# Kernel optimization log

Hardware: AMD Instinct MI355X
Metric: run time of the kernel (lower is better)

Reference implementation:

```python
import jax, jax.numpy as jnp
import numpy as np

N_ITERS = 2
N_NODES = 50000
N_EDGES = 400000
NODE_DIM = 128
EDGE_DIM = 128
MLP_HIDDEN = 128


def _gru_cell(x, h, W_ih, W_hh, b_ih, b_hh):
    # torch.nn.GRUCell math. W_ih: [3H, in], W_hh: [3H, H]
    gi = x @ W_ih.T + b_ih
    gh = h @ W_hh.T + b_hh
    i_r, i_z, i_n = jnp.split(gi, 3, axis=-1)
    h_r, h_z, h_n = jnp.split(gh, 3, axis=-1)
    r = jax.nn.sigmoid(i_r + h_r)
    z = jax.nn.sigmoid(i_z + h_z)
    n = jnp.tanh(i_n + r * h_n)
    return (1.0 - z) * n + z * h


def _edge_softmax(logits, dst, num_nodes):
    # logits: [E], normalized over incoming edges of each dst node
    m = jax.ops.segment_max(logits, dst, num_segments=num_nodes)
    e = jnp.exp(logits - m[dst])
    s = jax.ops.segment_sum(e, dst, num_segments=num_nodes)
    return e / s[dst]


def setup_inputs() -> dict:
    key = jax.random.key(0)
    ks = jax.random.split(key, 20)
    s = 0.05
    inp = {
        'nf': jax.random.normal(ks[0], (N_NODES, NODE_DIM), jnp.float32),
        'ef': jax.random.normal(ks[1], (N_EDGES, EDGE_DIM), jnp.float32),
        'src': jax.random.randint(ks[2], (N_EDGES,), 0, N_NODES, jnp.int32),
        'dst': jax.random.randint(ks[3], (N_EDGES,), 0, N_NODES, jnp.int32),
        # edge GRUCell: input 2*node_dim -> hidden edge_dim
        'eW_ih': s * jax.random.normal(ks[4], (3 * EDGE_DIM, 2 * NODE_DIM), jnp.float32),
        'eW_hh': s * jax.random.normal(ks[5], (3 * EDGE_DIM, EDGE_DIM), jnp.float32),
        'eb_ih': s * jax.random.normal(ks[6], (3 * EDGE_DIM,), jnp.float32),
        'eb_hh': s * jax.random.normal(ks[7], (3 * EDGE_DIM,), jnp.float32),
        # node GRUCell: input edge_dim -> hidden node_dim
        'nW_ih': s * jax.random.normal(ks[8], (3 * NODE_DIM, EDGE_DIM), jnp.float32),
        'nW_hh': s * jax.random.normal(ks[9], (3 * NODE_DIM, NODE_DIM), jnp.float32),
        'nb_ih': s * jax.random.normal(ks[10], (3 * NODE_DIM,), jnp.float32),
        'nb_hh': s * jax.random.normal(ks[11], (3 * NODE_DIM,), jnp.float32),
        # attention MLP: edge_dim -> hidden -> 1
        'aW1': s * jax.random.normal(ks[12], (EDGE_DIM, MLP_HIDDEN), jnp.float32),
        'ab1': jnp.zeros((MLP_HIDDEN,), jnp.float32),
        'aW2': s * jax.random.normal(ks[13], (MLP_HIDDEN, 1), jnp.float32),
        'ab2': jnp.zeros((1,), jnp.float32),
    }
    return inp


def reference(nf, ef, src, dst, eW_ih, eW_hh, eb_ih, eb_hh,
              nW_ih, nW_hh, nb_ih, nb_hh, aW1, ab1, aW2, ab2):
    num_nodes = nf.shape[0]
    for _ in range(N_ITERS):
        # per-edge GRU update: input = [src_h ; dst_h], hidden = edge feature
        x_e = jnp.concatenate([nf[src], nf[dst]], axis=-1)  # [E, 2*node_dim]
        uef = _gru_cell(x_e, ef, eW_ih, eW_hh, eb_ih, eb_hh)  # [E, edge_dim]
        # attention MLP + edge softmax over destination neighborhoods
        logits = (jax.nn.relu(uef @ aW1 + ab1) @ aW2 + ab2)[:, 0]  # [E]
        attn = _edge_softmax(logits, dst, num_nodes)  # [E]
        # weighted scatter-sum aggregation to destination nodes
        agg_m = jax.ops.segment_sum(uef * attn[:, None], dst, num_segments=num_nodes)
        # node GRU update
        unf = _gru_cell(agg_m, nf, nW_ih, nW_hh, nb_ih, nb_hh)  # [N, node_dim]
        nf, ef = unf, uef
    return (nf, ef)
```

## Files before the change

### kernel.cpp

```cpp
#include <hip/hip_runtime.h>

#define NN 50000
#define NE 400000
#define DIM 128

typedef __bf16 bf16x8 __attribute__((ext_vector_type(8)));
typedef float f32x4 __attribute__((ext_vector_type(4)));
typedef unsigned short u16;

#define MFMA16 __builtin_amdgcn_mfma_f32_16x16x32_bf16

__device__ __forceinline__ u16 f2b(float f){ __bf16 b=(__bf16)f; return __builtin_bit_cast(u16,b); }
__device__ __forceinline__ float b2f(u16 h){ unsigned u = ((unsigned)h)<<16; return __builtin_bit_cast(float,u); }
__device__ __forceinline__ float sigm(float x){ return 1.0f/(1.0f+__expf(-x)); }
__device__ __forceinline__ float tanh_(float x){ float e=__expf(2.0f*x); return 1.0f-2.0f/(e+1.0f); }
__device__ __forceinline__ bf16x8 ldb8(const u16* p){ return *reinterpret_cast<const bf16x8*>(p); }

#define GLOAD_LDS(gp, lp) __builtin_amdgcn_global_load_lds( \
    (const __attribute__((address_space(1))) void*)(gp),    \
    (__attribute__((address_space(3))) void*)(lp), 16, 0, 0)

__global__ void f2b_kernel(const float* __restrict__ in, u16* __restrict__ out, int n4){
  int i = blockIdx.x*blockDim.x + threadIdx.x;
  int st = gridDim.x*blockDim.x;
  for (; i<n4; i+=st){
    float4 v = reinterpret_cast<const float4*>(in)[i];
    ushort4 o = { f2b(v.x), f2b(v.y), f2b(v.z), f2b(v.w) };
    reinterpret_cast<ushort4*>(out)[i] = o;
  }
}

__global__ void transpose128_kernel(const float* __restrict__ in, u16* __restrict__ out){
  int i = blockIdx.x*blockDim.x + threadIdx.x;
  int k = i>>7, n = i&127;
  out[n*128+k] = f2b(in[i]);
}

__global__ void zero_kernel(int* p, int n){
  int i = blockIdx.x*blockDim.x + threadIdx.x; if (i<n) p[i]=0;
}
__global__ void hist_kernel(const int* __restrict__ dst, int* __restrict__ counts, int n){
  int i = blockIdx.x*blockDim.x + threadIdx.x; if (i<n) atomicAdd(&counts[dst[i]],1);
}
__global__ void scan_kernel(const int* __restrict__ counts, int* __restrict__ rowp,
                            int* __restrict__ cursor, int n){
  __shared__ int buf[1024];
  __shared__ int run;
  const int t = threadIdx.x;
  if (t==0) run = 0;
  __syncthreads();
  for (int base=0; base<n; base+=1024){
    int v = (base+t<n) ? counts[base+t] : 0;
    buf[t]=v; __syncthreads();
    for (int off=1; off<1024; off<<=1){
      int x = (t>=off) ? buf[t-off] : 0;
      __syncthreads();
      buf[t]+=x; __syncthreads();
    }
    int incl = buf[t];
    int br = run;
    __syncthreads();
    if (base+t<n){ int ex = br+incl-v; rowp[base+t]=ex; cursor[base+t]=ex; }
    if (t==1023) run = br+incl;
    __syncthreads();
  }
  if (t==0) rowp[n]=run;
}
__global__ void scatter_kernel(const int* __restrict__ dst, int* __restrict__ cursor,
                               int* __restrict__ eids, int n){
  int i = blockIdx.x*blockDim.x + threadIdx.x;
  if (i<n){ int p = atomicAdd(&cursor[dst[i]],1); eids[p]=i; }
}

__global__ __launch_bounds__(512, 4)
void edge_kernel(const int* __restrict__ src, const int* __restrict__ dst,
                 const u16* __restrict__ nfb, u16* __restrict__ efb,
                 const u16* __restrict__ Wih, const u16* __restrict__ Whh,
                 const float* __restrict__ bih, const float* __restrict__ bhh,
                 const u16* __restrict__ aW1T, const float* __restrict__ ab1,
                 const float* __restrict__ aW2, const float* __restrict__ ab2,
                 float* __restrict__ logits, float* __restrict__ ef32out)
{
  __shared__ __align__(16) u16 wbuf[36*512];
  const int wave = threadIdx.x>>6, lane = threadIdx.x&63;
  const int r16 = lane&15, kq = lane>>4;
  const long base = (long)blockIdx.x*128 + wave*16;
  const long e = base + r16;

  auto stage = [&](int c){
    if (c < 8){
      for (int f = wave; f < 36; f += 8){
        const u16* g;
        if (f < 24){ const int gt = f>>3, s = f&7;
          g = Wih + (long)(gt*128 + c*16 + r16)*256 + s*32 + kq*8; }
        else { const int q = f-24, gt = q>>2, s = q&3;
          g = Whh + (long)(gt*128 + c*16 + r16)*128 + s*32 + kq*8; }
        GLOAD_LDS(g, wbuf + f*512);
      }
    } else {
      for (int f = wave; f < 32; f += 8){
        const int t = f>>2, s = f&3;
        GLOAD_LDS(aW1T + (long)(t*16 + r16)*128 + s*32 + kq*8, wbuf + f*512);
      }
    }
  };

  const u16* sp = nfb + (long)src[e]*DIM;
  const u16* dp = nfb + (long)dst[e]*DIM;
  const u16* ep = efb + e*DIM;
  bf16x8 ag[8], ae[4];
#pragma unroll
  for (int s=0;s<4;++s){
    ag[s]   = ldb8(sp + s*32 + kq*8);
    ag[s+4] = ldb8(dp + s*32 + kq*8);
    ae[s]   = ldb8(ep + s*32 + kq*8);
  }
  stage(0);
  __syncthreads();

  u16*  ebase = efb + (base + kq*4)*DIM + r16;
  float* fbase = ef32out ? ef32out + (base + kq*4)*DIM + r16 : nullptr;
  const float* bi0 = bih + r16;
  const float* bh0 = bhh + r16;

  const f32x4 vzero = {0.f,0.f,0.f,0.f};
  const u16* lbase = wbuf + lane*8;

#pragma unroll 1
  for (int c=0;c<8;++c){
    const int c16 = c*16;
    const float bir=bi0[c16], biz=bi0[c16+DIM], bin=bi0[c16+2*DIM];
    const float bhr=bh0[c16], bhz=bh0[c16+DIM], bhn=bh0[c16+2*DIM];
    float h0p[4];
#pragma unroll
    for (int r=0;r<4;++r) h0p[r] = b2f(ebase[r*DIM + c16]);

    f32x4 ar=vzero, az=vzero, an=vzero, hr=vzero, hz=vzero, hn=vzero;
#pragma unroll
    for (int s=0;s<8;++s){
      ar = MFMA16(ag[s], ldb8(lbase + ( s   )*512), ar,0,0,0);
      az = MFMA16(ag[s], ldb8(lbase + ( 8+s )*512), az,0,0,0);
      an = MFMA16(ag[s], ldb8(lbase + (16+s )*512), an,0,0,0);
    }
#pragma unroll
    for (int s=0;s<4;++s){
      hr = MFMA16(ae[s], ldb8(lbase + (24+s)*512), hr,0,0,0);
      hz = MFMA16(ae[s], ldb8(lbase + (28+s)*512), hz,0,0,0);
      hn = MFMA16(ae[s], ldb8(lbase + (32+s)*512), hn,0,0,0);
    }
    __syncthreads();
    stage(c+1);
    float uv[4];
#pragma unroll
    for (int r=0;r<4;++r){
      float rg = sigm(ar[r]+bir + hr[r]+bhr);
      float zg = sigm(az[r]+biz + hz[r]+bhz);
      float ng = tanh_(an[r]+bin + rg*(hn[r]+bhn));
      float u  = (1.0f-zg)*ng + zg*h0p[r];
      ebase[r*DIM + c16] = f2b(u);
      uv[r] = u;
    }
    if (fbase){
#pragma unroll
      for (int r=0;r<4;++r) fbase[r*DIM + c16] = uv[r];
    }
    __syncthreads();
  }

  bf16x8 ua[4];
#pragma unroll
  for (int s=0;s<4;++s) ua[s] = ldb8(ep + s*32 + kq*8);
  float part[4] = {0.f,0.f,0.f,0.f};
#pragma unroll 1
  for (int t=0;t<8;++t){
    f32x4 h = vzero;
#pragma unroll
    for (int s=0;s<4;++s)
      h = MFMA16(ua[s], ldb8(lbase + (t*4+s)*512), h,0,0,0);
    const int cc = t*16 + r16;
    const float b1 = ab1[cc], w2 = aW2[cc];
#pragma unroll
    for (int r=0;r<4;++r) part[r] += fmaxf(h[r]+b1, 0.f)*w2;
  }
#pragma unroll
  for (int off=1; off<16; off<<=1){
#pragma unroll
    for (int r=0;r<4;++r) part[r] += __shfl_xor(part[r], off, 64);
  }
  if (r16==0){
    const float b2v = ab2[0];
#pragma unroll
    for (int r=0;r<4;++r) logits[base + kq*4 + r] = part[r] + b2v;
  }
}

__global__ __launch_bounds__(256)
void agg_kernel(const int* __restrict__ rowp, const int* __restrict__ eids,
                const float* __restrict__ logits, const u16* __restrict__ uefb,
                u16* __restrict__ aggb)
{
  const int wave = threadIdx.x>>6, lane = threadIdx.x&63;
  const int v = blockIdx.x*4 + wave;
  if (v>=NN) return;
  const int p0 = rowp[v], deg = rowp[v+1]-p0;
  float ax=0.f, ay=0.f;
  if (deg>0){
    float mx = -__builtin_inff();
    for (int i=lane; i<deg; i+=64) mx = fmaxf(mx, logits[eids[p0+i]]);
#pragma unroll
    for (int off=32; off; off>>=1) mx = fmaxf(mx, __shfl_xor(mx, off, 64));
    float ss = 0.f;
    for (int i=lane; i<deg; i+=64) ss += __expf(logits[eids[p0+i]] - mx);
#pragma unroll
    for (int off=32; off; off>>=1) ss += __shfl_xor(ss, off, 64);
    const float inv = 1.0f/ss;
    int i = 0;
    for (; i+2<=deg; i+=2){
      const int e0 = eids[p0+i], e1 = eids[p0+i+1];
      const float l0 = logits[e0], l1 = logits[e1];
      const unsigned q0 = *reinterpret_cast<const unsigned*>(uefb + (long)e0*DIM + lane*2);
      const unsigned q1 = *reinterpret_cast<const unsigned*>(uefb + (long)e1*DIM + lane*2);
      const float a0 = __expf(l0-mx)*inv, a1 = __expf(l1-mx)*inv;
      ax += a0*b2f((u16)q0) + a1*b2f((u16)q1);
      ay += a0*b2f((u16)(q0>>16)) + a1*b2f((u16)(q1>>16));
    }
    if (i<deg){
      const int e0 = eids[p0+i];
      const float a0 = __expf(logits[e0]-mx)*inv;
      const unsigned q0 = *reinterpret_cast<const unsigned*>(uefb + (long)e0*DIM + lane*2);
      ax += a0*b2f((u16)q0);
      ay += a0*b2f((u16)(q0>>16));
    }
  }
  unsigned pack = (unsigned)f2b(ax) | ((unsigned)f2b(ay)<<16);
  *reinterpret_cast<unsigned*>(aggb + (long)v*DIM + lane*2) = pack;
}

__global__ __launch_bounds__(512, 4)
void node_kernel(const u16* __restrict__ aggb, u16* __restrict__ nfb,
                 const float* nf32, float* unf32,
                 const u16* __restrict__ Wih, const u16* __restrict__ Whh,
                 const float* __restrict__ bih, const float* __restrict__ bhh)
{
  __shared__ __align__(16) u16 wbuf[2*24*512];
  const int wave = threadIdx.x>>6, lane = threadIdx.x&63;
  const int r16 = lane&15, kq = lane>>4;
  const long tbase = (long)blockIdx.x*128 + wave*16;
  const long v = tbase + r16;
  const long vcl = (v < NN) ? v : (NN-1);

  auto stage = [&](int c){
    if (c >= 8) return;
    u16* bufp = wbuf + (c&1)*24*512;
    for (int f = wave; f < 24; f += 8){
      const u16* g;
      if (f < 12){ const int gt = f>>2, s = f&3;
        g = Wih + (long)(gt*128 + c*16 + r16)*128 + s*32 + kq*8; }
      else { const int q = f-12, gt = q>>2, s = q&3;
        g = Whh + (long)(gt*128 + c*16 + r16)*128 + s*32 + kq*8; }
      GLOAD_LDS(g, bufp + f*512);
    }
  };

  bf16x8 xa[4], ha[4];
#pragma unroll
  for (int s=0;s<4;++s){
    xa[s] = ldb8(aggb + vcl*DIM + s*32 + kq*8);
    ha[s] = ldb8(nfb  + vcl*DIM + s*32 + kq*8);
  }
  stage(0);
  __syncthreads();

  const f32x4 vzero = {0.f,0.f,0.f,0.f};

#pragma unroll 1
  for (int c=0;c<8;++c){
    stage(c+1);
    const int oc = c*16 + r16;
    const float bir=bih[oc], biz=bih[DIM+oc], bin=bih[2*DIM+oc];
    const float bhr=bhh[oc], bhz=bhh[DIM+oc], bhn=bhh[2*DIM+oc];
    float h0p[4];
#pragma unroll
    for (int r=0;r<4;++r){
      const long rr = tbase + kq*4 + r;
      h0p[r] = (rr < NN) ? nf32[rr*DIM+oc] : 0.f;
    }
    const u16* lb = wbuf + (c&1)*24*512 + lane*8;
    f32x4 ar=vzero, az=vzero, an=vzero, hr=vzero, hz=vzero, hn=vzero;
#pragma unroll
    for (int s=0;s<4;++s){
      ar=MFMA16(xa[s], ldb8(lb + ( s   )*512), ar,0,0,0);
      az=MFMA16(xa[s], ldb8(lb + ( 4+s)*512), az,0,0,0);
      an=MFMA16(xa[s], ldb8(lb + ( 8+s)*512), an,0,0,0);
      hr=MFMA16(ha[s], ldb8(lb + (12+s)*512), hr,0,0,0);
      hz=MFMA16(ha[s], ldb8(lb + (16+s)*512), hz,0,0,0);
      hn=MFMA16(ha[s], ldb8(lb + (20+s)*512), hn,0,0,0);
    }
#pragma unroll
    for (int r=0;r<4;++r){
      const long rr = tbase + kq*4 + r;
      if (rr < NN){
        float rg = sigm(ar[r]+bir + hr[r]+bhr);
        float zg = sigm(az[r]+biz + hz[r]+bhz);
        float ng = tanh_(an[r]+bin + rg*(hn[r]+bhn));
        float u  = (1.0f-zg)*ng + zg*h0p[r];
        unf32[rr*DIM+oc] = u;
        nfb[rr*DIM+oc] = f2b(u);
      }
    }
    __syncthreads();
  }
}

extern "C" void kernel_launch(void* const* d_in, const int* in_sizes, int n_in,
                              void* d_out, int out_size, void* d_ws, size_t ws_size,
                              hipStream_t stream)
{
  const float* nf_in = (const float*)d_in[0];
  const float* ef_in = (const float*)d_in[1];
  const int*   src   = (const int*)d_in[2];
  const int*   dst   = (const int*)d_in[3];
  const float* eWih  = (const float*)d_in[4];
  const float* eWhh  = (const float*)d_in[5];
  const float* ebih  = (const float*)d_in[6];
  const float* ebhh  = (const float*)d_in[7];
  const float* nWih  = (const float*)d_in[8];
  const float* nWhh  = (const float*)d_in[9];
  const float* nbih  = (const float*)d_in[10];
  const float* nbhh  = (const float*)d_in[11];
  const float* aW1   = (const float*)d_in[12];
  const float* ab1   = (const float*)d_in[13];
  const float* aW2   = (const float*)d_in[14];
  const float* ab2   = (const float*)d_in[15];

  float* nf_out = (float*)d_out;
  float* ef_out = nf_out + (size_t)NN*DIM;

  char* p = (char*)d_ws;
  auto carve = [&](size_t bytes)->void*{ void* r = (void*)p; p += (bytes + 255) & ~(size_t)255; return r; };
  u16* efb    = (u16*)carve((size_t)NE*DIM*2);
  u16* nfb    = (u16*)carve((size_t)NN*DIM*2);
  u16* aggb   = (u16*)carve((size_t)NN*DIM*2);
  float* logits = (float*)carve((size_t)NE*4);
  int* eids   = (int*)carve((size_t)NE*4);
  int* counts = (int*)carve((size_t)NN*4);
  int* rowp   = (int*)carve((size_t)(NN+1)*4);
  int* cursor = (int*)carve((size_t)NN*4);
  u16* bWih   = (u16*)carve((size_t)384*256*2);
  u16* bWhh   = (u16*)carve((size_t)384*128*2);
  u16* bnWih  = (u16*)carve((size_t)384*128*2);
  u16* bnWhh  = (u16*)carve((size_t)384*128*2);
  u16* baW1T  = (u16*)carve((size_t)128*128*2);

  f2b_kernel<<<2048,256,0,stream>>>(nf_in, nfb, NN*DIM/4);
  f2b_kernel<<<2048,256,0,stream>>>(ef_in, efb, NE*DIM/4);
  f2b_kernel<<<96,256,0,stream>>>(eWih, bWih, 384*256/4);
  f2b_kernel<<<48,256,0,stream>>>(eWhh, bWhh, 384*128/4);
  f2b_kernel<<<48,256,0,stream>>>(nWih, bnWih, 384*128/4);
  f2b_kernel<<<48,256,0,stream>>>(nWhh, bnWhh, 384*128/4);
  transpose128_kernel<<<64,256,0,stream>>>(aW1, baW1T);

  zero_kernel<<<(NN+255)/256,256,0,stream>>>(counts, NN);
  hist_kernel<<<(NE+255)/256,256,0,stream>>>(dst, counts, NE);
  scan_kernel<<<1,1024,0,stream>>>(counts, rowp, cursor, NN);
  scatter_kernel<<<(NE+255)/256,256,0,stream>>>(dst, cursor, eids, NE);

  for (int it=0; it<2; ++it){
    const float* nf_cur = (it==0) ? nf_in : nf_out;
    float* efout32 = (it==1) ? ef_out : nullptr;
    edge_kernel<<<NE/128,512,0,stream>>>(src, dst, nfb, efb,
                                         bWih, bWhh, ebih, ebhh,
                                         baW1T, ab1, aW2, ab2, logits, efout32);
    agg_kernel<<<(NN+3)/4,256,0,stream>>>(rowp, eids, logits, efb, aggb);
    node_kernel<<<(NN+127)/128,512,0,stream>>>(aggb, nfb, nf_cur, nf_out,
                                               bnWih, bnWhh, nbih, nbhh);
  }
}
```

Measured before the change: 902.9 us.

## Process two 16-edge M-tiles per wave in edge kernel to reuse LDS weight fragments

Each wave now handles 32 edges as two 16-row MFMA tiles, so every weight fragment read from LDS feeds two MFMAs. The block shrinks to 4 waves of 256 threads while still covering 128 edges, and the staging loops are adjusted to match. The r and z gate accumulators for the input and hidden projections are merged, so only the n gate keeps separate input and hidden sums. This halves LDS reads per MFMA, but it raises register pressure and lowers the number of waves per block.

```diff
diff --git a/kernel.cpp b/kernel.cpp
--- a/kernel.cpp
+++ b/kernel.cpp
@@ -72,7 +72,7 @@
   if (i<n){ int p = atomicAdd(&cursor[dst[i]],1); eids[p]=i; }
 }
 
-__global__ __launch_bounds__(512, 4)
+__global__ __launch_bounds__(256, 2)
 void edge_kernel(const int* __restrict__ src, const int* __restrict__ dst,
                  const u16* __restrict__ nfb, u16* __restrict__ efb,
                  const u16* __restrict__ Wih, const u16* __restrict__ Whh,
@@ -84,12 +84,11 @@
   __shared__ __align__(16) u16 wbuf[36*512];
   const int wave = threadIdx.x>>6, lane = threadIdx.x&63;
   const int r16 = lane&15, kq = lane>>4;
-  const long base = (long)blockIdx.x*128 + wave*16;
-  const long e = base + r16;
+  const long base = (long)blockIdx.x*128 + wave*32;
 
   auto stage = [&](int c){
     if (c < 8){
-      for (int f = wave; f < 36; f += 8){
+      for (int f = wave; f < 36; f += 4){
         const u16* g;
         if (f < 24){ const int gt = f>>3, s = f&7;
           g = Wih + (long)(gt*128 + c*16 + r16)*256 + s*32 + kq*8; }
@@ -98,22 +97,26 @@
         GLOAD_LDS(g, wbuf + f*512);
       }
     } else {
-      for (int f = wave; f < 32; f += 8){
+      for (int f = wave; f < 32; f += 4){
         const int t = f>>2, s = f&3;
         GLOAD_LDS(aW1T + (long)(t*16 + r16)*128 + s*32 + kq*8, wbuf + f*512);
       }
     }
   };
 
-  const u16* sp = nfb + (long)src[e]*DIM;
-  const u16* dp = nfb + (long)dst[e]*DIM;
-  const u16* ep = efb + e*DIM;
-  bf16x8 ag[8], ae[4];
-#pragma unroll
-  for (int s=0;s<4;++s){
-    ag[s]   = ldb8(sp + s*32 + kq*8);
-    ag[s+4] = ldb8(dp + s*32 + kq*8);
-    ae[s]   = ldb8(ep + s*32 + kq*8);
+  bf16x8 ag[2][8], ae[2][4];
+#pragma unroll
+  for (int m=0;m<2;++m){
+    const long e = base + m*16 + r16;
+    const u16* sp = nfb + (long)src[e]*DIM;
+    const u16* dp = nfb + (long)dst[e]*DIM;
+    const u16* ep = efb + e*DIM;
+#pragma unroll
+    for (int s=0;s<4;++s){
+      ag[m][s]   = ldb8(sp + s*32 + kq*8);
+      ag[m][s+4] = ldb8(dp + s*32 + kq*8);
+      ae[m][s]   = ldb8(ep + s*32 + kq*8);
+    }
   }
   stage(0);
   __syncthreads();
@@ -131,66 +134,93 @@
     const int c16 = c*16;
     const float bir=bi0[c16], biz=bi0[c16+DIM], bin=bi0[c16+2*DIM];
     const float bhr=bh0[c16], bhz=bh0[c16+DIM], bhn=bh0[c16+2*DIM];
-    float h0p[4];
-#pragma unroll
-    for (int r=0;r<4;++r) h0p[r] = b2f(ebase[r*DIM + c16]);
-
-    f32x4 ar=vzero, az=vzero, an=vzero, hr=vzero, hz=vzero, hn=vzero;
+    float h0p[2][4];
+#pragma unroll
+    for (int m=0;m<2;++m)
+#pragma unroll
+      for (int r=0;r<4;++r) h0p[m][r] = b2f(ebase[(m*16+r)*DIM + c16]);
+
+    f32x4 aR[2], aZ[2], aNi[2], aNh[2];
+#pragma unroll
+    for (int m=0;m<2;++m){ aR[m]=vzero; aZ[m]=vzero; aNi[m]=vzero; aNh[m]=vzero; }
 #pragma unroll
     for (int s=0;s<8;++s){
-      ar = MFMA16(ag[s], ldb8(lbase + ( s   )*512), ar,0,0,0);
-      az = MFMA16(ag[s], ldb8(lbase + ( 8+s )*512), az,0,0,0);
-      an = MFMA16(ag[s], ldb8(lbase + (16+s )*512), an,0,0,0);
+      bf16x8 b0 = ldb8(lbase + ( s   )*512);
+      bf16x8 b1 = ldb8(lbase + ( 8+s )*512);
+      bf16x8 b2 = ldb8(lbase + (16+s )*512);
+#pragma unroll
+      for (int m=0;m<2;++m){
+        aR[m]  = MFMA16(ag[m][s], b0, aR[m] ,0,0,0);
+        aZ[m]  = MFMA16(ag[m][s], b1, aZ[m] ,0,0,0);
+        aNi[m] = MFMA16(ag[m][s], b2, aNi[m],0,0,0);
+      }
     }
 #pragma unroll
     for (int s=0;s<4;++s){
-      hr = MFMA16(ae[s], ldb8(lbase + (24+s)*512), hr,0,0,0);
-      hz = MFMA16(ae[s], ldb8(lbase + (28+s)*512), hz,0,0,0);
-      hn = MFMA16(ae[s], ldb8(lbase + (32+s)*512), hn,0,0,0);
+      bf16x8 b0 = ldb8(lbase + (24+s)*512);
+      bf16x8 b1 = ldb8(lbase + (28+s)*512);
+      bf16x8 b2 = ldb8(lbase + (32+s)*512);
+#pragma unroll
+      for (int m=0;m<2;++m){
+        aR[m]  = MFMA16(ae[m][s], b0, aR[m] ,0,0,0);
+        aZ[m]  = MFMA16(ae[m][s], b1, aZ[m] ,0,0,0);
+        aNh[m] = MFMA16(ae[m][s], b2, aNh[m],0,0,0);
+      }
     }
     __syncthreads();
     stage(c+1);
-    float uv[4];
-#pragma unroll
-    for (int r=0;r<4;++r){
-      float rg = sigm(ar[r]+bir + hr[r]+bhr);
-      float zg = sigm(az[r]+biz + hz[r]+bhz);
-      float ng = tanh_(an[r]+bin + rg*(hn[r]+bhn));
-      float u  = (1.0f-zg)*ng + zg*h0p[r];
-      ebase[r*DIM + c16] = f2b(u);
-      uv[r] = u;
-    }
-    if (fbase){
-#pragma unroll
-      for (int r=0;r<4;++r) fbase[r*DIM + c16] = uv[r];
+#pragma unroll
+    for (int m=0;m<2;++m){
+#pragma unroll
+      for (int r=0;r<4;++r){
+        float rg = sigm(aR[m][r] + bir + bhr);
+        float zg = sigm(aZ[m][r] + biz + bhz);
+        float ng = tanh_(aNi[m][r] + bin + rg*(aNh[m][r] + bhn));
+        float u  = (1.0f-zg)*ng + zg*h0p[m][r];
+        ebase[(m*16+r)*DIM + c16] = f2b(u);
+        if (fbase) fbase[(m*16+r)*DIM + c16] = u;
+      }
     }
     __syncthreads();
   }
 
-  bf16x8 ua[4];
-#pragma unroll
-  for (int s=0;s<4;++s) ua[s] = ldb8(ep + s*32 + kq*8);
-  float part[4] = {0.f,0.f,0.f,0.f};
+  bf16x8 ua[2][4];
+#pragma unroll
+  for (int m=0;m<2;++m){
+    const u16* ep = efb + (base + m*16 + r16)*DIM;
+#pragma unroll
+    for (int s=0;s<4;++s) ua[m][s] = ldb8(ep + s*32 + kq*8);
+  }
+  float part[2][4] = {{0.f,0.f,0.f,0.f},{0.f,0.f,0.f,0.f}};
 #pragma unroll 1
   for (int t=0;t<8;++t){
-    f32x4 h = vzero;
-#pragma unroll
-    for (int s=0;s<4;++s)
-      h = MFMA16(ua[s], ldb8(lbase + (t*4+s)*512), h,0,0,0);
+    f32x4 h[2] = {vzero, vzero};
+#pragma unroll
+    for (int s=0;s<4;++s){
+      bf16x8 b = ldb8(lbase + (t*4+s)*512);
+#pragma unroll
+      for (int m=0;m<2;++m) h[m] = MFMA16(ua[m][s], b, h[m],0,0,0);
+    }
     const int cc = t*16 + r16;
     const float b1 = ab1[cc], w2 = aW2[cc];
 #pragma unroll
-    for (int r=0;r<4;++r) part[r] += fmaxf(h[r]+b1, 0.f)*w2;
+    for (int m=0;m<2;++m)
+#pragma unroll
+      for (int r=0;r<4;++r) part[m][r] += fmaxf(h[m][r]+b1, 0.f)*w2;
   }
 #pragma unroll
   for (int off=1; off<16; off<<=1){
 #pragma unroll
-    for (int r=0;r<4;++r) part[r] += __shfl_xor(part[r], off, 64);
+    for (int m=0;m<2;++m)
+#pragma unroll
+      for (int r=0;r<4;++r) part[m][r] += __shfl_xor(part[m][r], off, 64);
   }
   if (r16==0){
     const float b2v = ab2[0];
 #pragma unroll
-    for (int r=0;r<4;++r) logits[base + kq*4 + r] = part[r] + b2v;
+    for (int m=0;m<2;++m)
+#pragma unroll
+      for (int r=0;r<4;++r) logits[base + m*16 + kq*4 + r] = part[m][r] + b2v;
   }
 }
 
@@ -368,7 +398,7 @@
   for (int it=0; it<2; ++it){
     const float* nf_cur = (it==0) ? nf_in : nf_out;
     float* efout32 = (it==1) ? ef_out : nullptr;
-    edge_kernel<<<NE/128,512,0,stream>>>(src, dst, nfb, efb,
+    edge_kernel<<<NE/128,256,0,stream>>>(src, dst, nfb, efb,
                                          bWih, bWhh, ebih, ebhh,
                                          baW1T, ab1, aW2, ab2, logits, efout32);
     agg_kernel<<<(NN+3)/4,256,0,stream>>>(rowp, eids, logits, efb, aggb);
```

After: 923.9 us. 2.3% more time.

## Fuse edge softmax aggregation into edge kernel via atomic scatter

Applied to the files above, without the earlier changes.

Removes the CSR build (histogram, scan, scatter) and the separate aggregation kernel. The edge kernel now exponentiates its logit without max subtraction and atomically adds weighted edge features and the weight into fp32 per-node accumulators. The node kernel then divides by the accumulated denominator. This trades gather passes for 51M float atomics per iteration plus memsets, and drops max-stabilisation, which risks overflow for large logits.

```diff
diff --git a/kernel.cpp b/kernel.cpp
--- a/kernel.cpp
+++ b/kernel.cpp
@@ -36,42 +36,6 @@
   out[n*128+k] = f2b(in[i]);
 }
 
-__global__ void zero_kernel(int* p, int n){
-  int i = blockIdx.x*blockDim.x + threadIdx.x; if (i<n) p[i]=0;
-}
-__global__ void hist_kernel(const int* __restrict__ dst, int* __restrict__ counts, int n){
-  int i = blockIdx.x*blockDim.x + threadIdx.x; if (i<n) atomicAdd(&counts[dst[i]],1);
-}
-__global__ void scan_kernel(const int* __restrict__ counts, int* __restrict__ rowp,
-                            int* __restrict__ cursor, int n){
-  __shared__ int buf[1024];
-  __shared__ int run;
-  const int t = threadIdx.x;
-  if (t==0) run = 0;
-  __syncthreads();
-  for (int base=0; base<n; base+=1024){
-    int v = (base+t<n) ? counts[base+t] : 0;
-    buf[t]=v; __syncthreads();
-    for (int off=1; off<1024; off<<=1){
-      int x = (t>=off) ? buf[t-off] : 0;
-      __syncthreads();
-      buf[t]+=x; __syncthreads();
-    }
-    int incl = buf[t];
-    int br = run;
-    __syncthreads();
-    if (base+t<n){ int ex = br+incl-v; rowp[base+t]=ex; cursor[base+t]=ex; }
-    if (t==1023) run = br+incl;
-    __syncthreads();
-  }
-  if (t==0) rowp[n]=run;
-}
-__global__ void scatter_kernel(const int* __restrict__ dst, int* __restrict__ cursor,
-                               int* __restrict__ eids, int n){
-  int i = blockIdx.x*blockDim.x + threadIdx.x;
-  if (i<n){ int p = atomicAdd(&cursor[dst[i]],1); eids[p]=i; }
-}
-
 __global__ __launch_bounds__(512, 4)
 void edge_kernel(const int* __restrict__ src, const int* __restrict__ dst,
                  const u16* __restrict__ nfb, u16* __restrict__ efb,
@@ -79,7 +43,8 @@
                  const float* __restrict__ bih, const float* __restrict__ bhh,
                  const u16* __restrict__ aW1T, const float* __restrict__ ab1,
                  const float* __restrict__ aW2, const float* __restrict__ ab2,
-                 float* __restrict__ logits, float* __restrict__ ef32out)
+                 float* __restrict__ aggf, float* __restrict__ denom,
+                 float* __restrict__ ef32out)
 {
   __shared__ __align__(16) u16 wbuf[36*512];
   const int wave = threadIdx.x>>6, lane = threadIdx.x&63;
@@ -156,7 +121,7 @@
       float rg = sigm(ar[r]+bir + hr[r]+bhr);
       float zg = sigm(az[r]+biz + hz[r]+bhz);
       float ng = tanh_(an[r]+bin + rg*(hn[r]+bhn));
-      float u  = (1.0f-zg)*ng + zg*h0p[r];
+      float u  = ng + zg*(h0p[r]-ng);
       ebase[r*DIM + c16] = f2b(u);
       uv[r] = u;
     }
@@ -187,57 +152,29 @@
 #pragma unroll
     for (int r=0;r<4;++r) part[r] += __shfl_xor(part[r], off, 64);
   }
-  if (r16==0){
-    const float b2v = ab2[0];
-#pragma unroll
-    for (int r=0;r<4;++r) logits[base + kq*4 + r] = part[r] + b2v;
-  }
-}
-
-__global__ __launch_bounds__(256)
-void agg_kernel(const int* __restrict__ rowp, const int* __restrict__ eids,
-                const float* __restrict__ logits, const u16* __restrict__ uefb,
-                u16* __restrict__ aggb)
-{
-  const int wave = threadIdx.x>>6, lane = threadIdx.x&63;
-  const int v = blockIdx.x*4 + wave;
-  if (v>=NN) return;
-  const int p0 = rowp[v], deg = rowp[v+1]-p0;
-  float ax=0.f, ay=0.f;
-  if (deg>0){
-    float mx = -__builtin_inff();
-    for (int i=lane; i<deg; i+=64) mx = fmaxf(mx, logits[eids[p0+i]]);
-#pragma unroll
-    for (int off=32; off; off>>=1) mx = fmaxf(mx, __shfl_xor(mx, off, 64));
-    float ss = 0.f;
-    for (int i=lane; i<deg; i+=64) ss += __expf(logits[eids[p0+i]] - mx);
-#pragma unroll
-    for (int off=32; off; off>>=1) ss += __shfl_xor(ss, off, 64);
-    const float inv = 1.0f/ss;
-    int i = 0;
-    for (; i+2<=deg; i+=2){
-      const int e0 = eids[p0+i], e1 = eids[p0+i+1];
-      const float l0 = logits[e0], l1 = logits[e1];
-      const unsigned q0 = *reinterpret_cast<const unsigned*>(uefb + (long)e0*DIM + lane*2);
-      const unsigned q1 = *reinterpret_cast<const unsigned*>(uefb + (long)e1*DIM + lane*2);
-      const float a0 = __expf(l0-mx)*inv, a1 = __expf(l1-mx)*inv;
-      ax += a0*b2f((u16)q0) + a1*b2f((u16)q1);
-      ay += a0*b2f((u16)(q0>>16)) + a1*b2f((u16)(q1>>16));
-    }
-    if (i<deg){
-      const int e0 = eids[p0+i];
-      const float a0 = __expf(logits[e0]-mx)*inv;
-      const unsigned q0 = *reinterpret_cast<const unsigned*>(uefb + (long)e0*DIM + lane*2);
-      ax += a0*b2f((u16)q0);
-      ay += a0*b2f((u16)(q0>>16));
-    }
-  }
-  unsigned pack = (unsigned)f2b(ax) | ((unsigned)f2b(ay)<<16);
-  *reinterpret_cast<unsigned*>(aggb + (long)v*DIM + lane*2) = pack;
+  const int srcl = (r16>>2)<<4;
+  const float w0 = __shfl(part[0], srcl, 64);
+  const float w1 = __shfl(part[1], srcl, 64);
+  const float w2v = __shfl(part[2], srcl, 64);
+  const float w3 = __shfl(part[3], srcl, 64);
+  const int rr = r16&3;
+  float lg = (rr==0) ? w0 : (rr==1) ? w1 : (rr==2) ? w2v : w3;
+  const float w = __expf(lg + ab2[0]);
+
+  const int dn = dst[e];
+  float* ab = aggf + (long)dn*DIM + kq*8;
+#pragma unroll
+  for (int s=0;s<4;++s){
+#pragma unroll
+    for (int j=0;j<8;++j)
+      atomicAdd(ab + s*32 + j, w * (float)ua[s][j]);
+  }
+  if (kq==0) atomicAdd(denom + dn, w);
 }
 
 __global__ __launch_bounds__(512, 4)
-void node_kernel(const u16* __restrict__ aggb, u16* __restrict__ nfb,
+void node_kernel(const float* __restrict__ aggf, const float* __restrict__ denom,
+                 u16* __restrict__ nfb,
                  const float* nf32, float* unf32,
                  const u16* __restrict__ Wih, const u16* __restrict__ Whh,
                  const float* __restrict__ bih, const float* __restrict__ bhh)
@@ -262,11 +199,21 @@
     }
   };
 
+  const float dnm = denom[vcl];
+  const float inv = (dnm > 0.f) ? 1.0f/dnm : 0.f;
   bf16x8 xa[4], ha[4];
 #pragma unroll
   for (int s=0;s<4;++s){
-    xa[s] = ldb8(aggb + vcl*DIM + s*32 + kq*8);
-    ha[s] = ldb8(nfb  + vcl*DIM + s*32 + kq*8);
+    const float* af = aggf + vcl*DIM + s*32 + kq*8;
+    float4 f0 = *reinterpret_cast<const float4*>(af);
+    float4 f1 = *reinterpret_cast<const float4*>(af+4);
+    bf16x8 t;
+    t[0]=(__bf16)(f0.x*inv); t[1]=(__bf16)(f0.y*inv);
+    t[2]=(__bf16)(f0.z*inv); t[3]=(__bf16)(f0.w*inv);
+    t[4]=(__bf16)(f1.x*inv); t[5]=(__bf16)(f1.y*inv);
+    t[6]=(__bf16)(f1.z*inv); t[7]=(__bf16)(f1.w*inv);
+    xa[s] = t;
+    ha[s] = ldb8(nfb + vcl*DIM + s*32 + kq*8);
   }
   stage(0);
   __syncthreads();
@@ -282,8 +229,8 @@
     float h0p[4];
 #pragma unroll
     for (int r=0;r<4;++r){
-      const long rr = tbase + kq*4 + r;
-      h0p[r] = (rr < NN) ? nf32[rr*DIM+oc] : 0.f;
+      const long rrw = tbase + kq*4 + r;
+      h0p[r] = (rrw < NN) ? nf32[rrw*DIM+oc] : 0.f;
     }
     const u16* lb = wbuf + (c&1)*24*512 + lane*8;
     f32x4 ar=vzero, az=vzero, an=vzero, hr=vzero, hz=vzero, hn=vzero;
@@ -298,14 +245,14 @@
     }
 #pragma unroll
     for (int r=0;r<4;++r){
-      const long rr = tbase + kq*4 + r;
-      if (rr < NN){
+      const long rrw = tbase + kq*4 + r;
+      if (rrw < NN){
         float rg = sigm(ar[r]+bir + hr[r]+bhr);
         float zg = sigm(az[r]+biz + hz[r]+bhz);
         float ng = tanh_(an[r]+bin + rg*(hn[r]+bhn));
-        float u  = (1.0f-zg)*ng + zg*h0p[r];
-        unf32[rr*DIM+oc] = u;
-        nfb[rr*DIM+oc] = f2b(u);
+        float u  = ng + zg*(h0p[r]-ng);
+        unf32[rrw*DIM+oc] = u;
+        nfb[rrw*DIM+oc] = f2b(u);
       }
     }
     __syncthreads();
@@ -340,12 +287,8 @@
   auto carve = [&](size_t bytes)->void*{ void* r = (void*)p; p += (bytes + 255) & ~(size_t)255; return r; };
   u16* efb    = (u16*)carve((size_t)NE*DIM*2);
   u16* nfb    = (u16*)carve((size_t)NN*DIM*2);
-  u16* aggb   = (u16*)carve((size_t)NN*DIM*2);
-  float* logits = (float*)carve((size_t)NE*4);
-  int* eids   = (int*)carve((size_t)NE*4);
-  int* counts = (int*)carve((size_t)NN*4);
-  int* rowp   = (int*)carve((size_t)(NN+1)*4);
-  int* cursor = (int*)carve((size_t)NN*4);
+  float* aggf = (float*)carve((size_t)NN*DIM*4);
+  float* denom= (float*)carve((size_t)NN*4);
   u16* bWih   = (u16*)carve((size_t)384*256*2);
   u16* bWhh   = (u16*)carve((size_t)384*128*2);
   u16* bnWih  = (u16*)carve((size_t)384*128*2);
@@ -360,19 +303,16 @@
   f2b_kernel<<<48,256,0,stream>>>(nWhh, bnWhh, 384*128/4);
   transpose128_kernel<<<64,256,0,stream>>>(aW1, baW1T);
 
-  zero_kernel<<<(NN+255)/256,256,0,stream>>>(counts, NN);
-  hist_kernel<<<(NE+255)/256,256,0,stream>>>(dst, counts, NE);
-  scan_kernel<<<1,1024,0,stream>>>(counts, rowp, cursor, NN);
-  scatter_kernel<<<(NE+255)/256,256,0,stream>>>(dst, cursor, eids, NE);
-
   for (int it=0; it<2; ++it){
     const float* nf_cur = (it==0) ? nf_in : nf_out;
     float* efout32 = (it==1) ? ef_out : nullptr;
+    hipMemsetAsync(aggf, 0, (size_t)NN*DIM*4, stream);
+    hipMemsetAsync(denom, 0, (size_t)NN*4, stream);
     edge_kernel<<<NE/128,512,0,stream>>>(src, dst, nfb, efb,
                                          bWih, bWhh, ebih, ebhh,
-                                         baW1T, ab1, aW2, ab2, logits, efout32);
-    agg_kernel<<<(NN+3)/4,256,0,stream>>>(rowp, eids, logits, efb, aggb);
-    node_kernel<<<(NN+127)/128,512,0,stream>>>(aggb, nfb, nf_cur, nf_out,
+                                         baW1T, ab1, aW2, ab2,
+                                         aggf, denom, efout32);
+    node_kernel<<<(NN+127)/128,512,0,stream>>>(aggf, denom, nfb, nf_cur, nf_out,
                                                bnWih, bnWhh, nbih, nbhh);
   }
 }
```

Result: slower. 3.171 ms (+251.2%).

## Sort edges by destination, parallelize CSR scan, read Whh/aW1 from global

Applied to the files above, without the earlier changes.

Edges are permuted into destination-sorted order once, via permuted src/dst arrays and a gather of edge features. The aggregation kernel then reads logits and updated edge features contiguously instead of through eids indirection. The final fp32 edge output is scattered back to the original edge order. The single-block scan becomes a three-phase multi-block scan. Inside the edge kernel, Whh and aW1T are now read directly from global/L2 instead of being staged in LDS, which shrinks LDS use, and s_setprio is added around the MFMA section. The cost is scattered fp32 stores, extra setup kernels, and L2 traffic for the weight reads.

```diff
diff --git a/kernel.cpp b/kernel.cpp
--- a/kernel.cpp
+++ b/kernel.cpp
@@ -42,38 +42,56 @@
 __global__ void hist_kernel(const int* __restrict__ dst, int* __restrict__ counts, int n){
   int i = blockIdx.x*blockDim.x + threadIdx.x; if (i<n) atomicAdd(&counts[dst[i]],1);
 }
-__global__ void scan_kernel(const int* __restrict__ counts, int* __restrict__ rowp,
-                            int* __restrict__ cursor, int n){
+__global__ void scanA_kernel(const int* __restrict__ counts, int* __restrict__ rowp,
+                             int* __restrict__ bsum, int n){
   __shared__ int buf[1024];
-  __shared__ int run;
-  const int t = threadIdx.x;
-  if (t==0) run = 0;
-  __syncthreads();
-  for (int base=0; base<n; base+=1024){
-    int v = (base+t<n) ? counts[base+t] : 0;
-    buf[t]=v; __syncthreads();
-    for (int off=1; off<1024; off<<=1){
-      int x = (t>=off) ? buf[t-off] : 0;
-      __syncthreads();
-      buf[t]+=x; __syncthreads();
-    }
-    int incl = buf[t];
-    int br = run;
+  const int gid = blockIdx.x*1024 + threadIdx.x;
+  int v = (gid<n) ? counts[gid] : 0;
+  buf[threadIdx.x]=v; __syncthreads();
+  for (int off=1; off<1024; off<<=1){
+    int x = (threadIdx.x>=off) ? buf[threadIdx.x-off] : 0;
     __syncthreads();
-    if (base+t<n){ int ex = br+incl-v; rowp[base+t]=ex; cursor[base+t]=ex; }
-    if (t==1023) run = br+incl;
-    __syncthreads();
-  }
-  if (t==0) rowp[n]=run;
+    buf[threadIdx.x]+=x; __syncthreads();
+  }
+  if (gid<n) rowp[gid] = buf[threadIdx.x]-v;
+  if (threadIdx.x==1023) bsum[blockIdx.x]=buf[1023];
+}
+__global__ void scanB_kernel(int* bsum, int* rowp, int nb, int n){
+  if (threadIdx.x==0 && blockIdx.x==0){
+    int run=0;
+    for (int b=0;b<nb;++b){ int t=bsum[b]; bsum[b]=run; run+=t; }
+    rowp[n]=run;
+  }
+}
+__global__ void scanC_kernel(int* __restrict__ rowp, int* __restrict__ cursor,
+                             const int* __restrict__ bsum, int n){
+  const int gid = blockIdx.x*1024 + threadIdx.x;
+  if (gid<n){ int v = rowp[gid]+bsum[blockIdx.x]; rowp[gid]=v; cursor[gid]=v; }
 }
 __global__ void scatter_kernel(const int* __restrict__ dst, int* __restrict__ cursor,
                                int* __restrict__ eids, int n){
   int i = blockIdx.x*blockDim.x + threadIdx.x;
   if (i<n){ int p = atomicAdd(&cursor[dst[i]],1); eids[p]=i; }
 }
+__global__ void perm_kernel(const int* __restrict__ eids, const int* __restrict__ src,
+                            const int* __restrict__ dst, int* __restrict__ srcp,
+                            int* __restrict__ dstp, int n){
+  int i = blockIdx.x*blockDim.x + threadIdx.x;
+  if (i<n){ int e=eids[i]; srcp[i]=src[e]; dstp[i]=dst[e]; }
+}
+__global__ void efgather_kernel(const int* __restrict__ eids, const float* __restrict__ ef,
+                                u16* __restrict__ efb){
+  long i = (long)blockIdx.x*256 + threadIdx.x;
+  long pos = i>>5; int k4 = (int)(i&31);
+  long e = eids[pos];
+  float4 v = reinterpret_cast<const float4*>(ef + e*DIM)[k4];
+  ushort4 o = { f2b(v.x), f2b(v.y), f2b(v.z), f2b(v.w) };
+  reinterpret_cast<ushort4*>(efb + pos*DIM)[k4] = o;
+}
 
 __global__ __launch_bounds__(512, 4)
-void edge_kernel(const int* __restrict__ src, const int* __restrict__ dst,
+void edge_kernel(const int* __restrict__ srcp, const int* __restrict__ dstp,
+                 const int* __restrict__ eids,
                  const u16* __restrict__ nfb, u16* __restrict__ efb,
                  const u16* __restrict__ Wih, const u16* __restrict__ Whh,
                  const float* __restrict__ bih, const float* __restrict__ bhh,
@@ -81,32 +99,22 @@
                  const float* __restrict__ aW2, const float* __restrict__ ab2,
                  float* __restrict__ logits, float* __restrict__ ef32out)
 {
-  __shared__ __align__(16) u16 wbuf[36*512];
+  __shared__ __align__(16) u16 wbuf[24*512];
   const int wave = threadIdx.x>>6, lane = threadIdx.x&63;
   const int r16 = lane&15, kq = lane>>4;
   const long base = (long)blockIdx.x*128 + wave*16;
   const long e = base + r16;
 
   auto stage = [&](int c){
-    if (c < 8){
-      for (int f = wave; f < 36; f += 8){
-        const u16* g;
-        if (f < 24){ const int gt = f>>3, s = f&7;
-          g = Wih + (long)(gt*128 + c*16 + r16)*256 + s*32 + kq*8; }
-        else { const int q = f-24, gt = q>>2, s = q&3;
-          g = Whh + (long)(gt*128 + c*16 + r16)*128 + s*32 + kq*8; }
-        GLOAD_LDS(g, wbuf + f*512);
-      }
-    } else {
-      for (int f = wave; f < 32; f += 8){
-        const int t = f>>2, s = f&3;
-        GLOAD_LDS(aW1T + (long)(t*16 + r16)*128 + s*32 + kq*8, wbuf + f*512);
-      }
+    if (c >= 8) return;
+    for (int f = wave; f < 24; f += 8){
+      const int gt = f>>3, s = f&7;
+      GLOAD_LDS(Wih + (long)(gt*128 + c*16 + r16)*256 + s*32 + kq*8, wbuf + f*512);
     }
   };
 
-  const u16* sp = nfb + (long)src[e]*DIM;
-  const u16* dp = nfb + (long)dst[e]*DIM;
+  const u16* sp = nfb + (long)srcp[e]*DIM;
+  const u16* dp = nfb + (long)dstp[e]*DIM;
   const u16* ep = efb + e*DIM;
   bf16x8 ag[8], ae[4];
 #pragma unroll
@@ -115,11 +123,14 @@
     ag[s+4] = ldb8(dp + s*32 + kq*8);
     ae[s]   = ldb8(ep + s*32 + kq*8);
   }
+  int oe[4];
+#pragma unroll
+  for (int r=0;r<4;++r) oe[r] = eids[base + kq*4 + r];
+
   stage(0);
   __syncthreads();
 
-  u16*  ebase = efb + (base + kq*4)*DIM + r16;
-  float* fbase = ef32out ? ef32out + (base + kq*4)*DIM + r16 : nullptr;
+  u16* ebase = efb + (base + kq*4)*DIM + r16;
   const float* bi0 = bih + r16;
   const float* bh0 = bhh + r16;
 
@@ -135,7 +146,9 @@
 #pragma unroll
     for (int r=0;r<4;++r) h0p[r] = b2f(ebase[r*DIM + c16]);
 
+    const u16* vr = Whh + (long)(c16 + r16)*128 + kq*8;
     f32x4 ar=vzero, az=vzero, an=vzero, hr=vzero, hz=vzero, hn=vzero;
+    __builtin_amdgcn_s_setprio(1);
 #pragma unroll
     for (int s=0;s<8;++s){
       ar = MFMA16(ag[s], ldb8(lbase + ( s   )*512), ar,0,0,0);
@@ -144,10 +157,11 @@
     }
 #pragma unroll
     for (int s=0;s<4;++s){
-      hr = MFMA16(ae[s], ldb8(lbase + (24+s)*512), hr,0,0,0);
-      hz = MFMA16(ae[s], ldb8(lbase + (28+s)*512), hz,0,0,0);
-      hn = MFMA16(ae[s], ldb8(lbase + (32+s)*512), hn,0,0,0);
-    }
+      hr = MFMA16(ae[s], ldb8(vr + s*32),           hr,0,0,0);
+      hz = MFMA16(ae[s], ldb8(vr + s*32 + 128*128), hz,0,0,0);
+      hn = MFMA16(ae[s], ldb8(vr + s*32 + 256*128), hn,0,0,0);
+    }
+    __builtin_amdgcn_s_setprio(0);
     __syncthreads();
     stage(c+1);
     float uv[4];
@@ -156,13 +170,13 @@
       float rg = sigm(ar[r]+bir + hr[r]+bhr);
       float zg = sigm(az[r]+biz + hz[r]+bhz);
       float ng = tanh_(an[r]+bin + rg*(hn[r]+bhn));
-      float u  = (1.0f-zg)*ng + zg*h0p[r];
+      float u  = ng + zg*(h0p[r]-ng);
       ebase[r*DIM + c16] = f2b(u);
       uv[r] = u;
     }
-    if (fbase){
-#pragma unroll
-      for (int r=0;r<4;++r) fbase[r*DIM + c16] = uv[r];
+    if (ef32out){
+#pragma unroll
+      for (int r=0;r<4;++r) ef32out[(long)oe[r]*DIM + c16 + r16] = uv[r];
     }
     __syncthreads();
   }
@@ -176,7 +190,7 @@
     f32x4 h = vzero;
 #pragma unroll
     for (int s=0;s<4;++s)
-      h = MFMA16(ua[s], ldb8(lbase + (t*4+s)*512), h,0,0,0);
+      h = MFMA16(ua[s], ldb8(aW1T + (long)(t*16+r16)*128 + s*32 + kq*8), h,0,0,0);
     const int cc = t*16 + r16;
     const float b1 = ab1[cc], w2 = aW2[cc];
 #pragma unroll
@@ -195,39 +209,36 @@
 }
 
 __global__ __launch_bounds__(256)
-void agg_kernel(const int* __restrict__ rowp, const int* __restrict__ eids,
-                const float* __restrict__ logits, const u16* __restrict__ uefb,
-                u16* __restrict__ aggb)
+void agg_kernel(const int* __restrict__ rowp, const float* __restrict__ logits,
+                const u16* __restrict__ uefb, u16* __restrict__ aggb)
 {
   const int wave = threadIdx.x>>6, lane = threadIdx.x&63;
   const int v = blockIdx.x*4 + wave;
   if (v>=NN) return;
-  const int p0 = rowp[v], deg = rowp[v+1]-p0;
+  const int p0 = rowp[v], p1 = rowp[v+1], deg = p1-p0;
   float ax=0.f, ay=0.f;
   if (deg>0){
     float mx = -__builtin_inff();
-    for (int i=lane; i<deg; i+=64) mx = fmaxf(mx, logits[eids[p0+i]]);
+    for (int i=p0+lane; i<p1; i+=64) mx = fmaxf(mx, logits[i]);
 #pragma unroll
     for (int off=32; off; off>>=1) mx = fmaxf(mx, __shfl_xor(mx, off, 64));
     float ss = 0.f;
-    for (int i=lane; i<deg; i+=64) ss += __expf(logits[eids[p0+i]] - mx);
+    for (int i=p0+lane; i<p1; i+=64) ss += __expf(logits[i] - mx);
 #pragma unroll
     for (int off=32; off; off>>=1) ss += __shfl_xor(ss, off, 64);
     const float inv = 1.0f/ss;
-    int i = 0;
-    for (; i+2<=deg; i+=2){
-      const int e0 = eids[p0+i], e1 = eids[p0+i+1];
-      const float l0 = logits[e0], l1 = logits[e1];
-      const unsigned q0 = *reinterpret_cast<const unsigned*>(uefb + (long)e0*DIM + lane*2);
-      const unsigned q1 = *reinterpret_cast<const unsigned*>(uefb + (long)e1*DIM + lane*2);
+    int i = p0;
+    for (; i+2<=p1; i+=2){
+      const float l0 = logits[i], l1 = logits[i+1];
+      const unsigned q0 = *reinterpret_cast<const unsigned*>(uefb + (long)i*DIM + lane*2);
+      const unsigned q1 = *reinterpret_cast<const unsigned*>(uefb + (long)(i+1)*DIM + lane*2);
       const float a0 = __expf(l0-mx)*inv, a1 = __expf(l1-mx)*inv;
       ax += a0*b2f((u16)q0) + a1*b2f((u16)q1);
       ay += a0*b2f((u16)(q0>>16)) + a1*b2f((u16)(q1>>16));
     }
-    if (i<deg){
-      const int e0 = eids[p0+i];
-      const float a0 = __expf(logits[e0]-mx)*inv;
-      const unsigned q0 = *reinterpret_cast<const unsigned*>(uefb + (long)e0*DIM + lane*2);
+    if (i<p1){
+      const float a0 = __expf(logits[i]-mx)*inv;
+      const unsigned q0 = *reinterpret_cast<const unsigned*>(uefb + (long)i*DIM + lane*2);
       ax += a0*b2f((u16)q0);
       ay += a0*b2f((u16)(q0>>16));
     }
@@ -303,7 +314,7 @@
         float rg = sigm(ar[r]+bir + hr[r]+bhr);
         float zg = sigm(az[r]+biz + hz[r]+bhz);
         float ng = tanh_(an[r]+bin + rg*(hn[r]+bhn));
-        float u  = (1.0f-zg)*ng + zg*h0p[r];
+        float u  = ng + zg*(h0p[r]-ng);
         unf32[rr*DIM+oc] = u;
         nfb[rr*DIM+oc] = f2b(u);
       }
@@ -343,35 +354,43 @@
   u16* aggb   = (u16*)carve((size_t)NN*DIM*2);
   float* logits = (float*)carve((size_t)NE*4);
   int* eids   = (int*)carve((size_t)NE*4);
+  int* srcp   = (int*)carve((size_t)NE*4);
+  int* dstp   = (int*)carve((size_t)NE*4);
   int* counts = (int*)carve((size_t)NN*4);
   int* rowp   = (int*)carve((size_t)(NN+1)*4);
   int* cursor = (int*)carve((size_t)NN*4);
+  int* bsum   = (int*)carve((size_t)64*4);
   u16* bWih   = (u16*)carve((size_t)384*256*2);
   u16* bWhh   = (u16*)carve((size_t)384*128*2);
   u16* bnWih  = (u16*)carve((size_t)384*128*2);
   u16* bnWhh  = (u16*)carve((size_t)384*128*2);
   u16* baW1T  = (u16*)carve((size_t)128*128*2);
 
+  const int NB = (NN + 1023)/1024;
+
+  zero_kernel<<<(NN+255)/256,256,0,stream>>>(counts, NN);
+  hist_kernel<<<(NE+255)/256,256,0,stream>>>(dst, counts, NE);
+  scanA_kernel<<<NB,1024,0,stream>>>(counts, rowp, bsum, NN);
+  scanB_kernel<<<1,64,0,stream>>>(bsum, rowp, NB, NN);
+  scanC_kernel<<<NB,1024,0,stream>>>(rowp, cursor, bsum, NN);
+  scatter_kernel<<<(NE+255)/256,256,0,stream>>>(dst, cursor, eids, NE);
+  perm_kernel<<<(NE+255)/256,256,0,stream>>>(eids, src, dst, srcp, dstp, NE);
+
   f2b_kernel<<<2048,256,0,stream>>>(nf_in, nfb, NN*DIM/4);
-  f2b_kernel<<<2048,256,0,stream>>>(ef_in, efb, NE*DIM/4);
+  efgather_kernel<<<NE*32/256,256,0,stream>>>(eids, ef_in, efb);
   f2b_kernel<<<96,256,0,stream>>>(eWih, bWih, 384*256/4);
   f2b_kernel<<<48,256,0,stream>>>(eWhh, bWhh, 384*128/4);
   f2b_kernel<<<48,256,0,stream>>>(nWih, bnWih, 384*128/4);
   f2b_kernel<<<48,256,0,stream>>>(nWhh, bnWhh, 384*128/4);
   transpose128_kernel<<<64,256,0,stream>>>(aW1, baW1T);
 
-  zero_kernel<<<(NN+255)/256,256,0,stream>>>(counts, NN);
-  hist_kernel<<<(NE+255)/256,256,0,stream>>>(dst, counts, NE);
-  scan_kernel<<<1,1024,0,stream>>>(counts, rowp, cursor, NN);
-  scatter_kernel<<<(NE+255)/256,256,0,stream>>>(dst, cursor, eids, NE);
-
   for (int it=0; it<2; ++it){
     const float* nf_cur = (it==0) ? nf_in : nf_out;
     float* efout32 = (it==1) ? ef_out : nullptr;
-    edge_kernel<<<NE/128,512,0,stream>>>(src, dst, nfb, efb,
+    edge_kernel<<<NE/128,512,0,stream>>>(srcp, dstp, eids, nfb, efb,
                                          bWih, bWhh, ebih, ebhh,
                                          baW1T, ab1, aW2, ab2, logits, efout32);
-    agg_kernel<<<(NN+3)/4,256,0,stream>>>(rowp, eids, logits, efb, aggb);
+    agg_kernel<<<(NN+3)/4,256,0,stream>>>(rowp, logits, efb, aggb);
     node_kernel<<<(NN+127)/128,512,0,stream>>>(aggb, nfb, nf_cur, nf_out,
                                                bnWih, bnWhh, nbih, nbhh);
   }
```

New measurement: 1.357 ms. 1.5x slower.
